# Kernel tuning notes

Measured on AMD Instinct MI355X. Metric: run time of the kernel, lower is better.

Reference implementation:

```python
import jax, jax.numpy as jnp
import numpy as np

K = 4  # number of scan directions (hard-coded in the module)


def setup_inputs() -> dict:
    key = jax.random.key(0)
    ks = jax.random.split(key, 6)
    B, C, H, W = 2, 96, 64, 64
    N = 16                 # state_rank
    R = C // N             # delta_rank = 6
    x = jax.random.normal(ks[0], (B, C, H, W), dtype=jnp.float32)
    # x_proj: Linear(C -> R + 2N), stacked K times (identical init in source)
    w = jax.random.uniform(ks[1], (R + 2 * N, C), minval=-(C ** -0.5), maxval=C ** -0.5)
    x_proj_weights = jnp.broadcast_to(w, (K, R + 2 * N, C)).astype(jnp.float32)
    # delta_proj: Linear(R -> C) with uniform(+-R^-0.5) weight and special bias
    dw = jax.random.uniform(ks[2], (C, R), minval=-(R ** -0.5), maxval=R ** -0.5)
    delta_projs_weights = jnp.broadcast_to(dw, (K, C, R)).astype(jnp.float32)
    dt = jnp.exp(jax.random.uniform(ks[3], (C,)) * (np.log(0.1) - np.log(0.001)) + np.log(0.001))
    dt = jnp.clip(dt, 1e-4, None)
    inv_dt = dt + jnp.log(-jnp.expm1(-dt))  # inverse softplus
    delta_projs_bias = jnp.broadcast_to(inv_dt, (K, C)).astype(jnp.float32)
    # A_log: log(arange(1..N)) per channel, repeated K times and merged -> (K*C, N)
    A_log = jnp.broadcast_to(jnp.log(jnp.arange(1, N + 1, dtype=jnp.float32)), (K * C, N))
    Ds = jnp.ones((K * C,), dtype=jnp.float32)
    return {"x": x, "x_proj_weights": x_proj_weights,
            "delta_projs_weights": delta_projs_weights,
            "delta_projs_bias": delta_projs_bias,
            "A_log": A_log, "Ds": Ds}


def _forward(x, x_proj_weights, delta_projs_weights, delta_projs_bias, A_log, Ds):
    B, C, H, W = x.shape
    L = H * W
    N = A_log.shape[-1]
    D = K * C
    # --- get_x: 4 directional flattenings: row-major, col-major, and their reverses
    x_row = x.reshape(B, C, L)
    x_col = jnp.swapaxes(x, 2, 3).reshape(B, C, L)
    xs = jnp.stack([x_row, x_col], axis=1)                   # (B,2,C,L)
    xs = jnp.concatenate([xs, jnp.flip(xs, axis=-1)], axis=1)  # (B,4,C,L)
    # --- get_DBC
    x_dbc = jnp.einsum('bkcl,kdc->bkdl', xs, x_proj_weights)
    R = delta_projs_weights.shape[-1]
    deltas, Bs, Cs = jnp.split(x_dbc, [R, R + N], axis=2)    # (B,K,R,L),(B,K,N,L),(B,K,N,L)
    deltas = jnp.einsum('bkrl,kcr->bkcl', deltas, delta_projs_weights)
    delta = deltas.reshape(B, D, L)
    delta_bias = delta_projs_bias.reshape(-1)                # (D,)
    A = -jnp.exp(A_log)                                      # (D,N)
    u = xs.reshape(B, D, L)
    # --- selective scan (delta_softplus=True)
    delta = jax.nn.softplus(delta + delta_bias[None, :, None])   # (B,D,L)
    deltaA = jnp.exp(delta[..., None] * A[None, :, None, :])     # (B,D,L,N)
    Bt = jnp.swapaxes(Bs, -1, -2)                                # (B,K,L,N)
    du = (delta * u).reshape(B, K, C, L)
    dBu = (du[..., None] * Bt[:, :, None]).reshape(B, D, L, N)   # delta*B*u

    def comb(e1, e2):
        a1, b1 = e1
        a2, b2 = e2
        return (a1 * a2, a2 * b1 + b2)

    _, hs = jax.lax.associative_scan(comb, (deltaA, dBu), axis=2)  # states (B,D,L,N)
    hs = hs.reshape(B, K, C, L, N)
    y = jnp.einsum('bkcln,bknl->bkcl', hs, Cs).reshape(B, D, L)
    y = y + Ds[None, :, None] * u
    # --- reassemble 4 directions back to row-major order
    y = y.reshape(B, K, C, L)
    y2 = jnp.flip(y[:, 2:4], axis=-1)                            # (B,2,C,L)
    y3 = jnp.swapaxes(y[:, 1].reshape(B, C, W, H), 2, 3).reshape(B, C, L)
    y4 = jnp.swapaxes(y2[:, 1].reshape(B, C, W, H), 2, 3).reshape(B, C, L)
    return (y[:, 0], y2[:, 0], y3, y4)


def reference(x, x_proj_weights, delta_projs_weights, delta_projs_bias, A_log, Ds):
    return _forward(x, x_proj_weights, delta_projs_weights, delta_projs_bias, A_log, Ds)
```

## Files before the change

### kernel.cpp

```cpp
#include <hip/hip_runtime.h>
#include <math.h>

#define B_ 2
#define C_ 96
#define L_ 4096
#define N_ 16
#define R_ 6
#define K_ 4
#define D38 38
#define D40 40
#define CMROW 257

typedef unsigned short ushort_t;
typedef unsigned int uint_t;

__device__ __forceinline__ uint_t bf16rtn(float f) {
    uint_t u = __float_as_uint(f);
    return (u + 0x7FFFu + ((u >> 16) & 1u)) >> 16;
}
__device__ __forceinline__ float bflo(uint_t p) { return __uint_as_float(p << 16); }
__device__ __forceinline__ float bfhi(uint_t p) { return __uint_as_float(p & 0xFFFF0000u); }

#define GETC(v, jj) ((jj) == 0 ? (v).x : (jj) == 1 ? (v).y : (jj) == 2 ? (v).z : (v).w)

__device__ __forceinline__ void rpow16(float r, float* p) {
    float r2 = r * r, r4 = r2 * r2, r8 = r4 * r4;
    p[0] = r;        p[1] = r2;       p[2] = r2 * r;   p[3] = r4;
    p[4] = r4 * r;   p[5] = r4 * r2;  p[6] = r4 * p[2]; p[7] = r8;
    p[8] = r8 * r;   p[9] = r8 * r2;  p[10] = r8 * p[2]; p[11] = r8 * r4;
    p[12] = r8 * p[4]; p[13] = r8 * p[5]; p[14] = r8 * p[6]; p[15] = r8 * r8;
}
__device__ __forceinline__ void unpack16(uint4 a, uint4 b, float* o) {
    o[0] = bflo(a.x);  o[1] = bfhi(a.x);  o[2] = bflo(a.y);  o[3] = bfhi(a.y);
    o[4] = bflo(a.z);  o[5] = bfhi(a.z);  o[6] = bflo(a.w);  o[7] = bfhi(a.w);
    o[8] = bflo(b.x);  o[9] = bfhi(b.x);  o[10] = bflo(b.y); o[11] = bfhi(b.y);
    o[12] = bflo(b.z); o[13] = bfhi(b.z); o[14] = bflo(b.w); o[15] = bfhi(b.w);
}

__global__ __launch_bounds__(256) void prep_kernel(
    const float* __restrict__ w, const float* __restrict__ x,
    const float* __restrict__ A_log,
    float* __restrict__ wt, float* __restrict__ xT, int* __restrict__ flag)
{
    int blk = blockIdx.x;
    int tid = threadIdx.x;
    if (blk < 60) {
        int i = blk * 256 + tid;
        if (i < K_ * C_ * D40) {
            int k   = i / (C_ * D40);
            int rem = i % (C_ * D40);
            int cc  = rem / D40;
            int dd  = rem % D40;
            wt[i] = (dd < D38) ? w[((size_t)k * D38 + dd) * C_ + cc] : 0.f;
        }
    } else if (blk < 60 + B_ * C_) {
        __shared__ float t[64][65];
        int bc = blk - 60;
        const float* src = x  + (size_t)bc * L_;
        float*       dst = xT + (size_t)bc * L_;
        int r0  = tid >> 6;
        int col = tid & 63;
        #pragma unroll
        for (int rr = 0; rr < 16; ++rr) {
            int row = rr * 4 + r0;
            t[row][col] = src[row * 64 + col];
        }
        __syncthreads();
        #pragma unroll
        for (int rr = 0; rr < 16; ++rr) {
            int row = rr * 4 + r0;
            dst[row * 64 + col] = t[col][row];
        }
    } else {
        bool ok = true;
        for (int i = tid; i < K_ * C_ * N_; i += 256) {
            float a = __expf(A_log[i]);
            ok = ok && (fabsf(a - (float)((i & 15) + 1)) < 1e-3f);
        }
        __shared__ int sok[4];
        unsigned long long m = __ballot(ok);
        if ((tid & 63) == 0) sok[tid >> 6] = (m == 0xFFFFFFFFFFFFFFFFull) ? 1 : 0;
        __syncthreads();
        if (tid == 0) flag[0] = sok[0] & sok[1] & sok[2] & sok[3];
    }
}

__global__ __launch_bounds__(512) void proj_kernel(
    const float* __restrict__ x, const float* __restrict__ xT,
    const float* __restrict__ wt, const float* __restrict__ dpw,
    const float* __restrict__ dpb,
    float* __restrict__ ws_r,
    ushort_t* __restrict__ ws_Bm, ushort_t* __restrict__ ws_Cm)
{
    __shared__ float T2[2][64][41];

    int blk  = blockIdx.x;
    int bk   = blk & 7;
    int lt   = blk >> 3;
    int k    = bk & 3;
    int b    = bk >> 2;

    int tid  = threadIdx.x;
    int l0   = tid & 63;
    int dq_u = __builtin_amdgcn_readfirstlane((tid >> 6) & 3);
    int ch_u = __builtin_amdgcn_readfirstlane(tid >> 8);
    int base = dq_u * 10;

    int l = lt * 64 + l0;
    int m = (k >= 2) ? (L_ - 1 - l) : l;
    const float* srcb = ((k & 1) ? xT : x) + (size_t)b * C_ * L_;

    const float* wk = wt + k * C_ * D40 + base;
    float acc[10];
    #pragma unroll
    for (int t = 0; t < 10; ++t) acc[t] = 0.f;
    int c0 = ch_u * 48;
    #pragma unroll 4
    for (int cc = 0; cc < 48; ++cc) {
        int c = c0 + cc;
        float xv = srcb[(size_t)c * L_ + m];
        const float* wc = wk + c * D40;
        #pragma unroll
        for (int t = 0; t < 10; ++t) acc[t] = fmaf(xv, wc[t], acc[t]);
    }
    #pragma unroll
    for (int t = 0; t < 10; ++t) T2[ch_u][l0][base + t] = acc[t];
    __syncthreads();

    {
        int lq = tid >> 3, sub = tid & 7;
        int buf = sub >> 2, q = sub & 3;
        int col = R_ + buf * 16 + 4 * q;
        float v0 = T2[0][lq][col]     + T2[1][lq][col];
        float v1 = T2[0][lq][col + 1] + T2[1][lq][col + 1];
        float v2 = T2[0][lq][col + 2] + T2[1][lq][col + 2];
        float v3 = T2[0][lq][col + 3] + T2[1][lq][col + 3];
        uint_t p0 = bf16rtn(v0) | (bf16rtn(v1) << 16);
        uint_t p1 = bf16rtn(v2) | (bf16rtn(v3) << 16);
        int ll = lt * 64 + lq;
        int j = ll & 15, g = ll >> 4;
        size_t o = (size_t)bk * 16384 + j * 1024 + g * 4 + q;
        uint2* dst = (uint2*)(buf ? ws_Cm : ws_Bm);
        dst[o] = make_uint2(p0, p1);
    }

    float ar[R_];
    #pragma unroll
    for (int r = 0; r < R_; ++r) ar[r] = T2[0][l0][r] + T2[1][l0][r];
    float* rlt = ws_r + (size_t)bk * C_ * L_ + lt * 64 + l0;
    int cq_u = ch_u * 4 + dq_u;
    #pragma unroll 2
    for (int cc = 0; cc < 12; ++cc) {
        int c = cc * 8 + cq_u;
        const float* dc = dpw + (k * C_ + c) * R_;
        float s = dpb[k * C_ + c];
        #pragma unroll
        for (int r = 0; r < R_; ++r) s = fmaf(ar[r], dc[r], s);
        float em  = __expf(-fabsf(s));
        float inv = 1.0f / (1.0f + em);
        float rr  = (s > 0.f) ? (em * inv) : inv;
        rlt[(size_t)c * L_] = rr;
    }
}

__global__ __launch_bounds__(256) void scan_kernel(
    const float* __restrict__ ws_r,
    const float* __restrict__ x, const float* __restrict__ xT,
    const ushort_t* __restrict__ ws_Bm, const ushort_t* __restrict__ ws_Cm,
    const float* __restrict__ A_log, const float* __restrict__ Ds,
    const int* __restrict__ flagp, float* __restrict__ out)
{
    __shared__ float s_u[16 * CMROW];
    __shared__ float s_r[16 * CMROW];
    __shared__ float s_wR[4];
    __shared__ float s_wB[4][N_];

    int blk = blockIdx.x;
    int bk  = blk & 7;
    int c   = blk >> 3;
    int k   = bk & 3;
    int b   = bk >> 2;
    int chn = bk * C_ + c;
    int d   = k * C_ + c;

    int t    = threadIdx.x;
    int w    = t >> 6;
    int lane = t & 63;

    int fast = flagp[0];
    float A16[16];
    if (!fast) {
        #pragma unroll
        for (int n = 0; n < 16; ++n)
            A16[n] = -__expf(A_log[(size_t)d * N_ + n]);
    }

    const float* usrc = ((k & 1) ? xT : x) + ((size_t)b * C_ + c) * L_;
    {
        const float* rp = ws_r + (size_t)chn * L_;
        #pragma unroll
        for (int it = 0; it < 4; ++it) {
            int e = t * 4 + it * 1024;
            float4 vr = *(const float4*)(rp + e);
            float4 vu;
            if (k < 2) {
                vu = *(const float4*)(usrc + e);
            } else {
                float4 t4 = *(const float4*)(usrc + (L_ - 4 - e));
                vu = make_float4(t4.w, t4.z, t4.y, t4.x);
            }
            int gg = e >> 4, j0 = e & 15;
            #pragma unroll
            for (int jj = 0; jj < 4; ++jj) {
                s_u[(j0 + jj) * CMROW + gg] = GETC(vu, jj);
                s_r[(j0 + jj) * CMROW + gg] = GETC(vr, jj);
            }
        }
    }
    __syncthreads();

    int g = t;
    const uint4* B4 = (const uint4*)ws_Bm;
    const uint4* C4 = (const uint4*)ws_Cm;
    int ib = bk * 8192 + g * 2;

    float Rc = 1.f, Sc = 0.f;
    float Bc[16];
    #pragma unroll
    for (int n = 0; n < 16; ++n) Bc[n] = 0.f;

    if (fast) {
        #pragma unroll 4
        for (int j = 0; j < 16; ++j) {
            float r  = s_r[j * CMROW + g];
            float u  = s_u[j * CMROW + g];
            float dl = -__logf(fmaxf(r, 1e-30f));
            float du = dl * u;
            uint4 b0 = B4[ib + j * 512];
            uint4 b1 = B4[ib + j * 512 + 1];
            float bb[16]; unpack16(b0, b1, bb);
            float p[16]; rpow16(r, p);
            #pragma unroll
            for (int n = 0; n < 16; ++n)
                Bc[n] = fmaf(p[n], Bc[n], du * bb[n]);
            Rc *= r;
        }
    } else {
        #pragma unroll 1
        for (int j = 0; j < 16; ++j) {
            float r  = s_r[j * CMROW + g];
            float u  = s_u[j * CMROW + g];
            float dl = -__logf(fmaxf(r, 1e-30f));
            float du = dl * u;
            uint4 b0 = B4[ib + j * 512];
            uint4 b1 = B4[ib + j * 512 + 1];
            float bb[16]; unpack16(b0, b1, bb);
            #pragma unroll
            for (int n = 0; n < 16; ++n) {
                float a = __expf(dl * A16[n]);
                Bc[n] = fmaf(a, Bc[n], du * bb[n]);
            }
            Sc += dl;
        }
    }

    if (fast) {
        #pragma unroll
        for (int s = 1; s < 64; s <<= 1) {
            float pR = __shfl_up(Rc, s, 64);
            float pB[16];
            #pragma unroll
            for (int n = 0; n < 16; ++n) pB[n] = __shfl_up(Bc[n], s, 64);
            if (lane >= s) {
                float p[16]; rpow16(Rc, p);
                #pragma unroll
                for (int n = 0; n < 16; ++n) Bc[n] = fmaf(p[n], pB[n], Bc[n]);
                Rc *= pR;
            }
        }
    } else {
        #pragma unroll 1
        for (int s = 1; s < 64; s <<= 1) {
            float pS = __shfl_up(Sc, s, 64);
            float pB[16];
            #pragma unroll
            for (int n = 0; n < 16; ++n) pB[n] = __shfl_up(Bc[n], s, 64);
            if (lane >= s) {
                #pragma unroll
                for (int n = 0; n < 16; ++n) {
                    float a = __expf(A16[n] * Sc);
                    Bc[n] = fmaf(a, pB[n], Bc[n]);
                }
                Sc += pS;
            }
        }
    }

    if (lane == 63) {
        s_wR[w] = fast ? Rc : Sc;
        #pragma unroll
        for (int n = 0; n < 16; ++n) s_wB[w][n] = Bc[n];
    }
    __syncthreads();

    float h[16];
    #pragma unroll
    for (int n = 0; n < 16; ++n) h[n] = 0.f;
    if (fast) {
        for (int v = 0; v < w; ++v) {
            float p[16]; rpow16(s_wR[v], p);
            #pragma unroll
            for (int n = 0; n < 16; ++n) h[n] = fmaf(p[n], h[n], s_wB[v][n]);
        }
        float pR = __shfl_up(Rc, 1, 64);
        float pB[16];
        #pragma unroll
        for (int n = 0; n < 16; ++n) pB[n] = __shfl_up(Bc[n], 1, 64);
        if (lane > 0) {
            float p[16]; rpow16(pR, p);
            #pragma unroll
            for (int n = 0; n < 16; ++n) h[n] = fmaf(p[n], h[n], pB[n]);
        }
    } else {
        #pragma unroll 1
        for (int v = 0; v < w; ++v) {
            float Sv = s_wR[v];
            #pragma unroll
            for (int n = 0; n < 16; ++n) {
                float a = __expf(A16[n] * Sv);
                h[n] = fmaf(a, h[n], s_wB[v][n]);
            }
        }
        float pS = __shfl_up(Sc, 1, 64);
        float pB[16];
        #pragma unroll
        for (int n = 0; n < 16; ++n) pB[n] = __shfl_up(Bc[n], 1, 64);
        if (lane > 0) {
            #pragma unroll
            for (int n = 0; n < 16; ++n) {
                float a = __expf(A16[n] * pS);
                h[n] = fmaf(a, h[n], pB[n]);
            }
        }
    }

    float Dd = Ds[d];
    int osel = (k == 0) ? 0 : (k == 2) ? 1 : (k == 1) ? 2 : 3;
    float* ob = out + ((size_t)osel * B_ + b) * ((size_t)C_ * L_) + (size_t)c * L_;
    int gl = g * 16;

    if (fast) {
        #pragma unroll
        for (int jq = 0; jq < 4; ++jq) {
            float yb0, yb1, yb2, yb3;
            #pragma unroll
            for (int jj = 0; jj < 4; ++jj) {
                int j = jq * 4 + jj;
                float r  = s_r[j * CMROW + g];
                float u  = s_u[j * CMROW + g];
                float dl = -__logf(fmaxf(r, 1e-30f));
                float du = dl * u;
                uint4 b0 = B4[ib + j * 512];
                uint4 b1 = B4[ib + j * 512 + 1];
                uint4 c0 = C4[ib + j * 512];
                uint4 c1 = C4[ib + j * 512 + 1];
                float bb[16]; unpack16(b0, b1, bb);
                float cc[16]; unpack16(c0, c1, cc);
                float p[16]; rpow16(r, p);
                float y = 0.f;
                #pragma unroll
                for (int n = 0; n < 16; ++n) {
                    h[n] = fmaf(p[n], h[n], du * bb[n]);
                    y = fmaf(h[n], cc[n], y);
                }
                y = fmaf(Dd, u, y);
                if (jj == 0) yb0 = y; else if (jj == 1) yb1 = y;
                else if (jj == 2) yb2 = y; else yb3 = y;
                if (k & 1) {
                    int l = gl + j;
                    int mm = (k == 1) ? l : (L_ - 1 - l);
                    ob[((mm & 63) << 6) | (mm >> 6)] = y;
                }
            }
            if (!(k & 1)) {
                if (k == 0) {
                    *(float4*)(ob + gl + jq * 4) = make_float4(yb0, yb1, yb2, yb3);
                } else {
                    *(float4*)(ob + (L_ - 4 - gl - jq * 4)) =
                        make_float4(yb3, yb2, yb1, yb0);
                }
            }
        }
    } else {
        #pragma unroll 1
        for (int j = 0; j < 16; ++j) {
            float r  = s_r[j * CMROW + g];
            float u  = s_u[j * CMROW + g];
            float dl = -__logf(fmaxf(r, 1e-30f));
            float du = dl * u;
            int l = gl + j;
            uint4 b0 = B4[ib + j * 512];
            uint4 b1 = B4[ib + j * 512 + 1];
            uint4 c0 = C4[ib + j * 512];
            uint4 c1 = C4[ib + j * 512 + 1];
            float bb[16]; unpack16(b0, b1, bb);
            float cc[16]; unpack16(c0, c1, cc);
            float y = 0.f;
            #pragma unroll
            for (int n = 0; n < 16; ++n) {
                float a = __expf(dl * A16[n]);
                h[n] = fmaf(a, h[n], du * bb[n]);
                y = fmaf(h[n], cc[n], y);
            }
            y = fmaf(Dd, u, y);
            int idx;
            if (k == 0)      idx = l;
            else if (k == 2) idx = L_ - 1 - l;
            else if (k == 1) idx = ((l & 63) << 6) | (l >> 6);
            else { int mm = L_ - 1 - l; idx = ((mm & 63) << 6) | (mm >> 6); }
            ob[idx] = y;
        }
    }
}

extern "C" void kernel_launch(void* const* d_in, const int* in_sizes, int n_in,
                              void* d_out, int out_size, void* d_ws, size_t ws_size,
                              hipStream_t stream) {
    const float* x     = (const float*)d_in[0];
    const float* xpw   = (const float*)d_in[1];
    const float* dpw   = (const float*)d_in[2];
    const float* dpb   = (const float*)d_in[3];
    const float* A_log = (const float*)d_in[4];
    const float* Ds    = (const float*)d_in[5];
    float* out = (float*)d_out;

    float* ws = (float*)d_ws;
    const size_t dL  = (size_t)B_ * K_ * C_ * L_;
    const size_t bcL = (size_t)B_ * K_ * L_ * N_;
    const size_t xL  = (size_t)B_ * C_ * L_;
    float*    ws_r  = ws;
    ushort_t* ws_Bm = (ushort_t*)(ws + dL);
    ushort_t* ws_Cm = ws_Bm + bcL;
    float*    ws_xT = ws + dL + bcL;
    float*    ws_Wt = ws_xT + xL;
    int*      ws_fl = (int*)(ws_Wt + (size_t)K_ * C_ * D40);

    prep_kernel<<<60 + B_ * C_ + 1, 256, 0, stream>>>(
        xpw, x, A_log, ws_Wt, ws_xT, ws_fl);
    proj_kernel<<<B_ * K_ * (L_ / 64), 512, 0, stream>>>(
        x, ws_xT, ws_Wt, dpw, dpb, ws_r, ws_Bm, ws_Cm);
    scan_kernel<<<B_ * K_ * C_, 256, 0, stream>>>(
        ws_r, x, ws_xT, ws_Bm, ws_Cm, A_log, Ds, ws_fl, out);
}
```

Before: 50.90 us.

## Split scan state across thread pairs, doubling scan block size

The scan kernel now uses 512 threads per block, with each pair of threads splitting the 16 state dimensions into two halves of 8. Each thread holds half the registers and loads one uint4 instead of two. The output dot product is combined with a shuffle-xor, and the warp prefix scan uses stride-2 shuffles. The goal is fewer registers per thread and more latency hiding through occupancy, at the cost of an extra shuffle per step and duplicated r/u/log work across each pair.

```diff
diff --git a/kernel.cpp b/kernel.cpp
--- a/kernel.cpp
+++ b/kernel.cpp
@@ -23,18 +23,17 @@
 
 #define GETC(v, jj) ((jj) == 0 ? (v).x : (jj) == 1 ? (v).y : (jj) == 2 ? (v).z : (v).w)
 
-__device__ __forceinline__ void rpow16(float r, float* p) {
-    float r2 = r * r, r4 = r2 * r2, r8 = r4 * r4;
-    p[0] = r;        p[1] = r2;       p[2] = r2 * r;   p[3] = r4;
-    p[4] = r4 * r;   p[5] = r4 * r2;  p[6] = r4 * p[2]; p[7] = r8;
-    p[8] = r8 * r;   p[9] = r8 * r2;  p[10] = r8 * p[2]; p[11] = r8 * r4;
-    p[12] = r8 * p[4]; p[13] = r8 * p[5]; p[14] = r8 * p[6]; p[15] = r8 * r8;
-}
-__device__ __forceinline__ void unpack16(uint4 a, uint4 b, float* o) {
-    o[0] = bflo(a.x);  o[1] = bfhi(a.x);  o[2] = bflo(a.y);  o[3] = bfhi(a.y);
-    o[4] = bflo(a.z);  o[5] = bfhi(a.z);  o[6] = bflo(a.w);  o[7] = bfhi(a.w);
-    o[8] = bflo(b.x);  o[9] = bfhi(b.x);  o[10] = bflo(b.y); o[11] = bfhi(b.y);
-    o[12] = bflo(b.z); o[13] = bfhi(b.z); o[14] = bflo(b.w); o[15] = bfhi(b.w);
+__device__ __forceinline__ void rpow8(float r, int hf, float* p) {
+    float r2 = r * r, r3 = r2 * r, r4 = r2 * r2;
+    p[0] = r;      p[1] = r2;     p[2] = r3;     p[3] = r4;
+    p[4] = r4 * r; p[5] = r4 * r2; p[6] = r4 * r3; p[7] = r4 * r4;
+    float sc = hf ? p[7] : 1.0f;
+    #pragma unroll
+    for (int e = 0; e < 8; ++e) p[e] *= sc;
+}
+__device__ __forceinline__ void unpack8(uint4 a, float* o) {
+    o[0] = bflo(a.x); o[1] = bfhi(a.x); o[2] = bflo(a.y); o[3] = bfhi(a.y);
+    o[4] = bflo(a.z); o[5] = bfhi(a.z); o[6] = bflo(a.w); o[7] = bfhi(a.w);
 }
 
 __global__ __launch_bounds__(256) void prep_kernel(
@@ -163,7 +162,7 @@
     }
 }
 
-__global__ __launch_bounds__(256) void scan_kernel(
+__global__ __launch_bounds__(512, 6) void scan_kernel(
     const float* __restrict__ ws_r,
     const float* __restrict__ x, const float* __restrict__ xT,
     const ushort_t* __restrict__ ws_Bm, const ushort_t* __restrict__ ws_Cm,
@@ -172,8 +171,8 @@
 {
     __shared__ float s_u[16 * CMROW];
     __shared__ float s_r[16 * CMROW];
-    __shared__ float s_wR[4];
-    __shared__ float s_wB[4][N_];
+    __shared__ float s_wR[8];
+    __shared__ float s_wB[8][N_];
 
     int blk = blockIdx.x;
     int bk  = blk & 7;
@@ -184,23 +183,26 @@
     int d   = k * C_ + c;
 
     int t    = threadIdx.x;
+    int hf   = t & 1;
+    int g    = t >> 1;
     int w    = t >> 6;
     int lane = t & 63;
+    int i    = lane >> 1;
 
     int fast = flagp[0];
-    float A16[16];
+    float A8[8];
     if (!fast) {
         #pragma unroll
-        for (int n = 0; n < 16; ++n)
-            A16[n] = -__expf(A_log[(size_t)d * N_ + n]);
+        for (int e = 0; e < 8; ++e)
+            A8[e] = -__expf(A_log[(size_t)d * N_ + 8 * hf + e]);
     }
 
     const float* usrc = ((k & 1) ? xT : x) + ((size_t)b * C_ + c) * L_;
     {
         const float* rp = ws_r + (size_t)chn * L_;
         #pragma unroll
-        for (int it = 0; it < 4; ++it) {
-            int e = t * 4 + it * 1024;
+        for (int it = 0; it < 2; ++it) {
+            int e = t * 4 + it * 2048;
             float4 vr = *(const float4*)(rp + e);
             float4 vu;
             if (k < 2) {
@@ -219,15 +221,14 @@
     }
     __syncthreads();
 
-    int g = t;
     const uint4* B4 = (const uint4*)ws_Bm;
     const uint4* C4 = (const uint4*)ws_Cm;
-    int ib = bk * 8192 + g * 2;
+    int ib = bk * 8192 + g * 2 + hf;
 
     float Rc = 1.f, Sc = 0.f;
-    float Bc[16];
-    #pragma unroll
-    for (int n = 0; n < 16; ++n) Bc[n] = 0.f;
+    float Bc[8];
+    #pragma unroll
+    for (int e = 0; e < 8; ++e) Bc[e] = 0.f;
 
     if (fast) {
         #pragma unroll 4
@@ -236,13 +237,12 @@
             float u  = s_u[j * CMROW + g];
             float dl = -__logf(fmaxf(r, 1e-30f));
             float du = dl * u;
-            uint4 b0 = B4[ib + j * 512];
-            uint4 b1 = B4[ib + j * 512 + 1];
-            float bb[16]; unpack16(b0, b1, bb);
-            float p[16]; rpow16(r, p);
-            #pragma unroll
-            for (int n = 0; n < 16; ++n)
-                Bc[n] = fmaf(p[n], Bc[n], du * bb[n]);
+            uint4 bv = B4[ib + j * 512];
+            float bb[8]; unpack8(bv, bb);
+            float p[8]; rpow8(r, hf, p);
+            #pragma unroll
+            for (int e = 0; e < 8; ++e)
+                Bc[e] = fmaf(p[e], Bc[e], du * bb[e]);
             Rc *= r;
         }
     } else {
@@ -252,13 +252,12 @@
             float u  = s_u[j * CMROW + g];
             float dl = -__logf(fmaxf(r, 1e-30f));
             float du = dl * u;
-            uint4 b0 = B4[ib + j * 512];
-            uint4 b1 = B4[ib + j * 512 + 1];
-            float bb[16]; unpack16(b0, b1, bb);
-            #pragma unroll
-            for (int n = 0; n < 16; ++n) {
-                float a = __expf(dl * A16[n]);
-                Bc[n] = fmaf(a, Bc[n], du * bb[n]);
+            uint4 bv = B4[ib + j * 512];
+            float bb[8]; unpack8(bv, bb);
+            #pragma unroll
+            for (int e = 0; e < 8; ++e) {
+                float a = __expf(dl * A8[e]);
+                Bc[e] = fmaf(a, Bc[e], du * bb[e]);
             }
             Sc += dl;
         }
@@ -266,80 +265,81 @@
 
     if (fast) {
         #pragma unroll
-        for (int s = 1; s < 64; s <<= 1) {
-            float pR = __shfl_up(Rc, s, 64);
-            float pB[16];
-            #pragma unroll
-            for (int n = 0; n < 16; ++n) pB[n] = __shfl_up(Bc[n], s, 64);
-            if (lane >= s) {
-                float p[16]; rpow16(Rc, p);
+        for (int s = 1; s < 32; s <<= 1) {
+            float pR = __shfl_up(Rc, 2 * s, 64);
+            float pB[8];
+            #pragma unroll
+            for (int e = 0; e < 8; ++e) pB[e] = __shfl_up(Bc[e], 2 * s, 64);
+            if (i >= s) {
+                float p[8]; rpow8(Rc, hf, p);
                 #pragma unroll
-                for (int n = 0; n < 16; ++n) Bc[n] = fmaf(p[n], pB[n], Bc[n]);
+                for (int e = 0; e < 8; ++e) Bc[e] = fmaf(p[e], pB[e], Bc[e]);
                 Rc *= pR;
             }
         }
     } else {
         #pragma unroll 1
-        for (int s = 1; s < 64; s <<= 1) {
-            float pS = __shfl_up(Sc, s, 64);
-            float pB[16];
-            #pragma unroll
-            for (int n = 0; n < 16; ++n) pB[n] = __shfl_up(Bc[n], s, 64);
-            if (lane >= s) {
+        for (int s = 1; s < 32; s <<= 1) {
+            float pS = __shfl_up(Sc, 2 * s, 64);
+            float pB[8];
+            #pragma unroll
+            for (int e = 0; e < 8; ++e) pB[e] = __shfl_up(Bc[e], 2 * s, 64);
+            if (i >= s) {
                 #pragma unroll
-                for (int n = 0; n < 16; ++n) {
-                    float a = __expf(A16[n] * Sc);
-                    Bc[n] = fmaf(a, pB[n], Bc[n]);
+                for (int e = 0; e < 8; ++e) {
+                    float a = __expf(A8[e] * Sc);
+                    Bc[e] = fmaf(a, pB[e], Bc[e]);
                 }
                 Sc += pS;
             }
         }
     }
 
-    if (lane == 63) {
-        s_wR[w] = fast ? Rc : Sc;
-        #pragma unroll
-        for (int n = 0; n < 16; ++n) s_wB[w][n] = Bc[n];
+    if (i == 31) {
+        if (hf == 0) s_wR[w] = fast ? Rc : Sc;
+        #pragma unroll
+        for (int e = 0; e < 8; ++e) s_wB[w][8 * hf + e] = Bc[e];
     }
     __syncthreads();
 
-    float h[16];
-    #pragma unroll
-    for (int n = 0; n < 16; ++n) h[n] = 0.f;
+    float h[8];
+    #pragma unroll
+    for (int e = 0; e < 8; ++e) h[e] = 0.f;
     if (fast) {
+        #pragma unroll 1
         for (int v = 0; v < w; ++v) {
-            float p[16]; rpow16(s_wR[v], p);
-            #pragma unroll
-            for (int n = 0; n < 16; ++n) h[n] = fmaf(p[n], h[n], s_wB[v][n]);
-        }
-        float pR = __shfl_up(Rc, 1, 64);
-        float pB[16];
-        #pragma unroll
-        for (int n = 0; n < 16; ++n) pB[n] = __shfl_up(Bc[n], 1, 64);
-        if (lane > 0) {
-            float p[16]; rpow16(pR, p);
-            #pragma unroll
-            for (int n = 0; n < 16; ++n) h[n] = fmaf(p[n], h[n], pB[n]);
+            float p[8]; rpow8(s_wR[v], hf, p);
+            #pragma unroll
+            for (int e = 0; e < 8; ++e) h[e] = fmaf(p[e], h[e], s_wB[v][8 * hf + e]);
+        }
+        float pR = __shfl_up(Rc, 2, 64);
+        float pB[8];
+        #pragma unroll
+        for (int e = 0; e < 8; ++e) pB[e] = __shfl_up(Bc[e], 2, 64);
+        if (i > 0) {
+            float p[8]; rpow8(pR, hf, p);
+            #pragma unroll
+            for (int e = 0; e < 8; ++e) h[e] = fmaf(p[e], h[e], pB[e]);
         }
     } else {
         #pragma unroll 1
         for (int v = 0; v < w; ++v) {
             float Sv = s_wR[v];
             #pragma unroll
-            for (int n = 0; n < 16; ++n) {
-                float a = __expf(A16[n] * Sv);
-                h[n] = fmaf(a, h[n], s_wB[v][n]);
-            }
-        }
-        float pS = __shfl_up(Sc, 1, 64);
-        float pB[16];
-        #pragma unroll
-        for (int n = 0; n < 16; ++n) pB[n] = __shfl_up(Bc[n], 1, 64);
-        if (lane > 0) {
-            #pragma unroll
-            for (int n = 0; n < 16; ++n) {
-                float a = __expf(A16[n] * pS);
-                h[n] = fmaf(a, h[n], pB[n]);
+            for (int e = 0; e < 8; ++e) {
+                float a = __expf(A8[e] * Sv);
+                h[e] = fmaf(a, h[e], s_wB[v][8 * hf + e]);
+            }
+        }
+        float pS = __shfl_up(Sc, 2, 64);
+        float pB[8];
+        #pragma unroll
+        for (int e = 0; e < 8; ++e) pB[e] = __shfl_up(Bc[e], 2, 64);
+        if (i > 0) {
+            #pragma unroll
+            for (int e = 0; e < 8; ++e) {
+                float a = __expf(A8[e] * pS);
+                h[e] = fmaf(a, h[e], pB[e]);
             }
         }
     }
@@ -360,29 +360,28 @@
                 float u  = s_u[j * CMROW + g];
                 float dl = -__logf(fmaxf(r, 1e-30f));
                 float du = dl * u;
-                uint4 b0 = B4[ib + j * 512];
-                uint4 b1 = B4[ib + j * 512 + 1];
-                uint4 c0 = C4[ib + j * 512];
-                uint4 c1 = C4[ib + j * 512 + 1];
-                float bb[16]; unpack16(b0, b1, bb);
-                float cc[16]; unpack16(c0, c1, cc);
-                float p[16]; rpow16(r, p);
+                uint4 bv = B4[ib + j * 512];
+                uint4 cv = C4[ib + j * 512];
+                float bb[8]; unpack8(bv, bb);
+                float cc[8]; unpack8(cv, cc);
+                float p[8]; rpow8(r, hf, p);
                 float y = 0.f;
                 #pragma unroll
-                for (int n = 0; n < 16; ++n) {
-                    h[n] = fmaf(p[n], h[n], du * bb[n]);
-                    y = fmaf(h[n], cc[n], y);
+                for (int e = 0; e < 8; ++e) {
+                    h[e] = fmaf(p[e], h[e], du * bb[e]);
+                    y = fmaf(h[e], cc[e], y);
                 }
+                y += __shfl_xor(y, 1, 64);
                 y = fmaf(Dd, u, y);
                 if (jj == 0) yb0 = y; else if (jj == 1) yb1 = y;
                 else if (jj == 2) yb2 = y; else yb3 = y;
-                if (k & 1) {
+                if ((k & 1) && hf == 0) {
                     int l = gl + j;
                     int mm = (k == 1) ? l : (L_ - 1 - l);
                     ob[((mm & 63) << 6) | (mm >> 6)] = y;
                 }
             }
-            if (!(k & 1)) {
+            if (!(k & 1) && hf == 0) {
                 if (k == 0) {
                     *(float4*)(ob + gl + jq * 4) = make_float4(yb0, yb1, yb2, yb3);
                 } else {
@@ -399,26 +398,27 @@
             float dl = -__logf(fmaxf(r, 1e-30f));
             float du = dl * u;
             int l = gl + j;
-            uint4 b0 = B4[ib + j * 512];
-            uint4 b1 = B4[ib + j * 512 + 1];
-            uint4 c0 = C4[ib + j * 512];
-            uint4 c1 = C4[ib + j * 512 + 1];
-            float bb[16]; unpack16(b0, b1, bb);
-            float cc[16]; unpack16(c0, c1, cc);
+            uint4 bv = B4[ib + j * 512];
+            uint4 cv = C4[ib + j * 512];
+            float bb[8]; unpack8(bv, bb);
+            float cc[8]; unpack8(cv, cc);
             float y = 0.f;
             #pragma unroll
-            for (int n = 0; n < 16; ++n) {
-                float a = __expf(dl * A16[n]);
-                h[n] = fmaf(a, h[n], du * bb[n]);
-                y = fmaf(h[n], cc[n], y);
-            }
-            y = fmaf(Dd, u, y);
-            int idx;
-            if (k == 0)      idx = l;
-            else if (k == 2) idx = L_ - 1 - l;
-            else if (k == 1) idx = ((l & 63) << 6) | (l >> 6);
-            else { int mm = L_ - 1 - l; idx = ((mm & 63) << 6) | (mm >> 6); }
-            ob[idx] = y;
+            for (int e = 0; e < 8; ++e) {
+                float a = __expf(dl * A8[e]);
+                h[e] = fmaf(a, h[e], du * bb[e]);
+                y = fmaf(h[e], cc[e], y);
+            }
+            y += __shfl_xor(y, 1, 64);
+            if (hf == 0) {
+                y = fmaf(Dd, u, y);
+                int idx;
+                if (k == 0)      idx = l;
+                else if (k == 2) idx = L_ - 1 - l;
+                else if (k == 1) idx = ((l & 63) << 6) | (l >> 6);
+                else { int mm = L_ - 1 - l; idx = ((mm & 63) << 6) | (mm >> 6); }
+                ob[idx] = y;
+            }
         }
     }
 }
@@ -449,6 +449,6 @@
         xpw, x, A_log, ws_Wt, ws_xT, ws_fl);
     proj_kernel<<<B_ * K_ * (L_ / 64), 512, 0, stream>>>(
         x, ws_xT, ws_Wt, dpw, dpb, ws_r, ws_Bm, ws_Cm);
-    scan_kernel<<<B_ * K_ * C_, 256, 0, stream>>>(
+    scan_kernel<<<B_ * K_ * C_, 512, 0, stream>>>(
         ws_r, x, ws_xT, ws_Bm, ws_Cm, A_log, Ds, ws_fl, out);
 }
```

New measurement: 53.78 us. 5.7% more time.
